# Kernel optimization log

Measured on AMD Instinct MI355X. Metric: run time of the kernel, lower is better.

## Reference

```python
import jax, jax.numpy as jnp
import numpy as np

K = 3            # kernel_size
ZETA = 1e-3      # crf_zeta
NUM_ITER = 2     # crf_num_iter
TOL = 0.0        # tolerance


def unfold3(x):
    """torch.nn.Unfold(3, stride=1, padding=1): [B,C,H,W] -> [B,C,9,H*W].
    Channel-major, kernel positions row-major (matches torch ordering)."""
    B, C, H, W = x.shape
    xp = jnp.pad(x, ((0, 0), (0, 0), (1, 1), (1, 1)))
    patches = jnp.stack(
        [xp[:, :, i:i + H, j:j + W] for i in range(K) for j in range(K)], axis=2
    )  # [B,C,9,H,W]
    return patches.reshape(B, C, K * K, H * W)


def setup_inputs() -> dict:
    key = jax.random.key(0)
    k1, k2, k3 = jax.random.split(key, 3)
    B, C, H, W, D = 2, 3, 256, 704, 64
    # scale color to O(zeta) so the gaussian affinity kernel is non-degenerate
    color = jax.random.normal(k1, (B, C, H, W), dtype=jnp.float32) * ZETA
    feats = jax.random.normal(k2, (B, C, H, W), dtype=jnp.float32)  # unused by forward, kept for signature fidelity
    logits = jax.random.normal(k3, (B, D, H, W), dtype=jnp.float32)
    ws = jnp.full((1,), 0.015, dtype=jnp.float32)  # learned weight self.ws[0]
    return {"color": color, "feats": feats, "logits": logits, "ws": ws}


def reference(color, feats, logits, ws):
    B, C, H, W = color.shape
    D = logits.shape[1]
    HW = H * W

    # gaussian affinity kernel from guide image: [B, 9, HW]
    uc = unfold3(color)  # [B,C,9,HW]
    kernel = jnp.exp(-(((uc - color.reshape(B, C, 1, HW)) ** 2)
                       / (2.0 * ZETA ** 2)).sum(1))

    # label compatibility matrix miu: [D, D]
    idx = jnp.arange(D)
    miu = jnp.clip(jnp.abs(idx[:, None] - idx[None, :]).astype(jnp.float32) - TOL, 0.0)

    logits_flat = logits.reshape(B, D, HW)
    q = jax.nn.softmax(logits, axis=1)
    for _ in range(NUM_ITER):
        uq = unfold3(q)  # [B,D,9,HW]
        q_tilde = (uq * kernel[:, None]).sum(2) * ws  # [B,D,HW]
        q_hat = jnp.einsum('de,ben->bdn', miu, q_tilde)  # [B,D,HW]
        q = jax.nn.softmax(logits_flat - q_hat, axis=1).reshape(B, D, H, W)
    return q
```

## Files before the change

### kernel.cpp

```cpp
#include <hip/hip_runtime.h>
#include <hip/hip_fp16.h>

#define HH 256
#define WW 704
#define DD 64
#define CC 3
#define BB 2
#define HWN (HH * WW)

#define TY 8
#define TX 16
#define RY0 12
#define RX0 20
#define NP0 (RY0 * RX0)
#define RY1 10
#define RX1 18
#define NP1 (RY1 * RX1)
#define NTX (WW / TX)
#define NTY (HH / TY)
#define NTILES (NTX * NTY)

static constexpr float INV2Z2 = 1.0f / (2.0f * 1e-3f * 1e-3f);

__global__ __launch_bounds__(256) void affinity_kernel(
    const float* __restrict__ color, const float* __restrict__ wsp,
    float* __restrict__ kaff)
{
    int n = blockIdx.x * 256 + threadIdx.x;
    int b = blockIdx.y;
    int h = n / WW, w = n - h * WW;
    float wsv = wsp[0];

    const float* cb = color + (size_t)b * CC * HWN + n;
    float c0 = cb[0], c1 = cb[HWN], c2 = cb[2 * HWN];
    bool hm = h > 0, hp = h < HH - 1, wm = w > 0, wp = w < WW - 1;

    float* kb = kaff + (size_t)b * 9 * HWN + n;
#pragma unroll
    for (int dh = -1; dh <= 1; ++dh) {
#pragma unroll
        for (int dw = -1; dw <= 1; ++dw) {
            int k = (dh + 1) * 3 + (dw + 1);
            bool valid = (dh < 0 ? hm : (dh > 0 ? hp : true)) &&
                         (dw < 0 ? wm : (dw > 0 ? wp : true));
            int off = valid ? (dh * WW + dw) : 0;
            float u0 = valid ? cb[off] : 0.f;
            float u1 = valid ? cb[HWN + off] : 0.f;
            float u2 = valid ? cb[2 * HWN + off] : 0.f;
            float d0 = u0 - c0, d1 = u1 - c1, d2 = u2 - c2;
            float ss = d0 * d0 + d1 * d1 + d2 * d2;
            kb[(size_t)k * HWN] = wsv * __expf(-ss * INV2Z2);
        }
    }
}

__device__ __forceinline__ void acc_tap(const unsigned* q, int p0, int cg,
                                        __half2 kh, __half2* tv2) {
    int ia = p0 * 32 + ((cg * 8) ^ ((p0 & 7) << 2));
    int ib = ia ^ 4;
    const __half2* qa = (const __half2*)&q[ia];
    const __half2* qb = (const __half2*)&q[ib];
    tv2[0] = __hfma2(kh, qa[0], tv2[0]);
    tv2[1] = __hfma2(kh, qa[1], tv2[1]);
    tv2[2] = __hfma2(kh, qa[2], tv2[2]);
    tv2[3] = __hfma2(kh, qa[3], tv2[3]);
    tv2[4] = __hfma2(kh, qb[0], tv2[4]);
    tv2[5] = __hfma2(kh, qb[1], tv2[5]);
    tv2[6] = __hfma2(kh, qb[2], tv2[6]);
    tv2[7] = __hfma2(kh, qb[3], tv2[7]);
}

__device__ __forceinline__ void pack_px(const float* u, float scale,
                                        uint4& a, uint4& bu) {
    __half2* pa = (__half2*)&a;
    __half2* pb = (__half2*)&bu;
    pa[0] = __floats2half2_rn(u[0]  * scale, u[1]  * scale);
    pa[1] = __floats2half2_rn(u[2]  * scale, u[3]  * scale);
    pa[2] = __floats2half2_rn(u[4]  * scale, u[5]  * scale);
    pa[3] = __floats2half2_rn(u[6]  * scale, u[7]  * scale);
    pb[0] = __floats2half2_rn(u[8]  * scale, u[9]  * scale);
    pb[1] = __floats2half2_rn(u[10] * scale, u[11] * scale);
    pb[2] = __floats2half2_rn(u[12] * scale, u[13] * scale);
    pb[3] = __floats2half2_rn(u[14] * scale, u[15] * scale);
}

__device__ __forceinline__ void st_raw(unsigned* q, int p, int cg,
                                       uint4 a, uint4 bu) {
    int ia = p * 32 + ((cg * 8) ^ ((p & 7) << 2));
    *(uint4*)&q[ia] = a;
    *(uint4*)&q[ia ^ 4] = bu;
}

__device__ __forceinline__ void st_px(unsigned* q, int p, int cg,
                                      const float* u, float scale) {
    uint4 a, bu;
    pack_px(u, scale, a, bu);
    st_raw(q, p, cg, a, bu);
}

__device__ __forceinline__ void scan4(float Aloc, float Bloc, int pxl, int cg,
                                      float& Ar, float& Br, float& T, float& E) {
    float A0 = __shfl(Aloc, pxl),      A1 = __shfl(Aloc, pxl + 16),
          A2 = __shfl(Aloc, pxl + 32), A3 = __shfl(Aloc, pxl + 48);
    float B0 = __shfl(Bloc, pxl),      B1 = __shfl(Bloc, pxl + 16),
          B2 = __shfl(Bloc, pxl + 32), B3 = __shfl(Bloc, pxl + 48);
    T = A0 + A1 + A2 + A3;  E = B0 + B1 + B2 + B3;
    Ar = 0.f; Br = 0.f;
    if (cg > 0) { Ar += A0; Br += B0; }
    if (cg > 1) { Ar += A1; Br += B1; }
    if (cg > 2) { Ar += A2; Br += B2; }
}

__device__ __forceinline__ float finish_px(float* tv, const float* lg,
                                           int pxl, int cg) {
    float Aloc = 0.f, Bloc = 0.f;
#pragma unroll
    for (int i = 0; i < 16; ++i) {
        float e = (float)(cg * 16 + i);
        Aloc += tv[i]; Bloc += e * tv[i];
    }
    float Ar, Br, T, E;
    scan4(Aloc, Bloc, pxl, cg, Ar, Br, T, E);
    float s = 0.f;
#pragma unroll
    for (int i = 0; i < 16; ++i) {
        float e = (float)(cg * 16 + i);
        Ar += tv[i]; Br += e * tv[i];
        float v = lg[(size_t)i * HWN] - (2.f * (e * Ar - Br) + E - e * T);
        tv[i] = __expf(v); s += tv[i];
    }
    s += __shfl_xor(s, 16);
    s += __shfl_xor(s, 32);
    return 1.f / s;
}

__device__ __forceinline__ void load_k(const float* kfb, int n, int gy, int gx,
                                       float* k) {
#pragma unroll
    for (int j = 0; j < 9; ++j) k[j] = kfb[(size_t)j * HWN + n];
    if (gy <= 0)      { k[0] = k[1] = k[2] = 0.f; }
    if (gy >= HH - 1) { k[6] = k[7] = k[8] = 0.f; }
    if (gx <= 0)      { k[0] = k[3] = k[6] = 0.f; }
    if (gx >= WW - 1) { k[2] = k[5] = k[8] = 0.f; }
}

__device__ __forceinline__ void stencil9(const unsigned* qs, int rowstride,
                                         int py, int px, int cg,
                                         const float* k, float* tv) {
    __half2 tv2[8];
#pragma unroll
    for (int j = 0; j < 8; ++j) tv2[j] = __float2half2_rn(0.f);
    int base = (py + 1) * rowstride + (px + 1);
#pragma unroll
    for (int tap = 0; tap < 9; ++tap) {
        int dy = tap / 3 - 1, dx = tap - (tap / 3) * 3 - 1;
        acc_tap(qs, base + dy * rowstride + dx, cg, __float2half2_rn(k[tap]), tv2);
    }
#pragma unroll
    for (int j = 0; j < 8; ++j) {
        float2 f = __half22float2(tv2[j]);
        tv[2 * j] = f.x; tv[2 * j + 1] = f.y;
    }
}

__global__ __launch_bounds__(512) void fused_crf_kernel(
    const float* __restrict__ logits, const float* __restrict__ kaff,
    float* __restrict__ qout)
{
    __shared__ unsigned qs[NP0 * 32];

    const int t = threadIdx.x;
    const int lane = t & 63;
    const int wv = t >> 6;
    const int pxl = lane & 15;
    const int cg = lane >> 4;
    const int b = blockIdx.y;
    const int tid16 = wv * 16 + pxl;

    const int bid = blockIdx.x;
    const int pb = (bid & 7) * (NTILES / 8) + (bid >> 3);
    const int tyr = pb / NTX, txc = pb - tyr * NTX;
    const int y0 = tyr * TY, x0 = txc * TX;

    const float* lgb = logits + ((size_t)b * DD + cg * 16) * HWN;
    const float* kfb = kaff + (size_t)b * 9 * HWN;

    for (int r = 0; r < 2; ++r) {
        int id = r * 128 + tid16;
        if (id < NP0) {
            int py = id / RX0, px = id - py * RX0;
            int gy = min(max(y0 - 2 + py, 0), HH - 1);
            int gx = min(max(x0 - 2 + px, 0), WW - 1);
            const float* lg = lgb + gy * WW + gx;
            float v[16];
            float s = 0.f;
#pragma unroll
            for (int i = 0; i < 16; ++i) {
                v[i] = __expf(lg[(size_t)i * HWN]);
                s += v[i];
            }
            s += __shfl_xor(s, 16);
            s += __shfl_xor(s, 32);
            st_px(qs, id, cg, v, 1.0f / s);
        }
    }
    __syncthreads();

    uint4 aA, buA;
    {
        int py = tid16 / RX1, px = tid16 - py * RX1;
        int gy = y0 - 1 + py, gx = x0 - 1 + px;
        int cy = min(max(gy, 0), HH - 1), cx = min(max(gx, 0), WW - 1);
        int n = cy * WW + cx;
        float k[9];
        load_k(kfb, n, gy, gx, k);
        float tv[16];
        stencil9(qs, RX0, py, px, cg, k, tv);
        float inv = finish_px(tv, lgb + n, pxl, cg);
        pack_px(tv, inv, aA, buA);
    }
    const int idB = 128 + tid16;
    const bool validB = idB < NP1;
    uint4 aB, buB;
    if (validB) {
        int py = idB / RX1, px = idB - py * RX1;
        int gy = y0 - 1 + py, gx = x0 - 1 + px;
        int cy = min(max(gy, 0), HH - 1), cx = min(max(gx, 0), WW - 1);
        int n = cy * WW + cx;
        float k[9];
        load_k(kfb, n, gy, gx, k);
        float tv[16];
        stencil9(qs, RX0, py, px, cg, k, tv);
        float inv = finish_px(tv, lgb + n, pxl, cg);
        pack_px(tv, inv, aB, buB);
    }
    __syncthreads();

    st_raw(qs, tid16, cg, aA, buA);
    if (validB) st_raw(qs, idB, cg, aB, buB);
    __syncthreads();

    {
        int py = tid16 >> 4, px = tid16 & 15;
        int gy = y0 + py, gx = x0 + px;
        int n = gy * WW + gx;

        float k[9];
        load_k(kfb, n, gy, gx, k);

        float tv[16];
        stencil9(qs, RX1, py, px, cg, k, tv);
        float inv = finish_px(tv, lgb + n, pxl, cg);

        float* qo = qout + ((size_t)b * DD + cg * 16) * HWN + n;
#pragma unroll
        for (int i = 0; i < 16; ++i) qo[(size_t)i * HWN] = tv[i] * inv;
    }
}

extern "C" void kernel_launch(void* const* d_in, const int* in_sizes, int n_in,
                              void* d_out, int out_size, void* d_ws, size_t ws_size,
                              hipStream_t stream) {
    const float* color  = (const float*)d_in[0];
    const float* logits = (const float*)d_in[2];
    const float* wsp    = (const float*)d_in[3];

    float* q_out = (float*)d_out;
    float* kaff  = (float*)d_ws;

    dim3 gridA(HWN / 256, BB);
    affinity_kernel<<<gridA, 256, 0, stream>>>(color, wsp, kaff);

    dim3 gridF(NTILES, BB);
    fused_crf_kernel<<<gridF, 512, 0, stream>>>(logits, kaff, q_out);
}
```

Measured before the change: 90.01 us.

## Replace per-iteration logits reloads with cached softmax times exp2 of message

Uses the identity softmax(logits - q_hat) ∝ softmax(logits) · exp(-q_hat). Both CRF iterations now multiply the initial fp16 softmax, already held in shared memory, by exp(-q_hat) instead of reloading 64 logits per pixel from global memory. The ws weight is pre-scaled by log2(e) so the exponent can use the hardware exp2 instruction. The centre q0 for the final stage is read from shared memory before the buffer is overwritten. This removes a large share of global read traffic, at the cost of using fp16-rounded q0 as the base, which loses some precision for very small probabilities.

```diff
diff --git a/kernel.cpp b/kernel.cpp
--- a/kernel.cpp
+++ b/kernel.cpp
@@ -21,6 +21,15 @@
 #define NTILES (NTX * NTY)
 
 static constexpr float INV2Z2 = 1.0f / (2.0f * 1e-3f * 1e-3f);
+static constexpr float LOG2E  = 1.4426950408889634f;
+
+__device__ __forceinline__ float fexp2(float x) {
+#if __has_builtin(__builtin_amdgcn_exp2f)
+    return __builtin_amdgcn_exp2f(x);
+#else
+    return __expf(x * 0.6931471805599453f);
+#endif
+}
 
 __global__ __launch_bounds__(256) void affinity_kernel(
     const float* __restrict__ color, const float* __restrict__ wsp,
@@ -29,7 +38,7 @@
     int n = blockIdx.x * 256 + threadIdx.x;
     int b = blockIdx.y;
     int h = n / WW, w = n - h * WW;
-    float wsv = wsp[0];
+    float wsv = wsp[0] * LOG2E;
 
     const float* cb = color + (size_t)b * CC * HWN + n;
     float c0 = cb[0], c1 = cb[HWN], c2 = cb[2 * HWN];
@@ -70,6 +79,28 @@
     tv2[7] = __hfma2(kh, qb[3], tv2[7]);
 }
 
+__device__ __forceinline__ void ld_raw(const unsigned* q, int p, int cg,
+                                       uint4& a, uint4& bu) {
+    int ia = p * 32 + ((cg * 8) ^ ((p & 7) << 2));
+    a  = *(const uint4*)&q[ia];
+    bu = *(const uint4*)&q[ia ^ 4];
+}
+
+__device__ __forceinline__ void unpack_px(uint4 a, uint4 bu, float* qc) {
+    const __half2* pa = (const __half2*)&a;
+    const __half2* pb = (const __half2*)&bu;
+#pragma unroll
+    for (int j = 0; j < 4; ++j) {
+        float2 f = __half22float2(pa[j]);
+        qc[2 * j] = f.x; qc[2 * j + 1] = f.y;
+    }
+#pragma unroll
+    for (int j = 0; j < 4; ++j) {
+        float2 f = __half22float2(pb[j]);
+        qc[8 + 2 * j] = f.x; qc[8 + 2 * j + 1] = f.y;
+    }
+}
+
 __device__ __forceinline__ void pack_px(const float* u, float scale,
                                         uint4& a, uint4& bu) {
     __half2* pa = (__half2*)&a;
@@ -111,8 +142,8 @@
     if (cg > 2) { Ar += A2; Br += B2; }
 }
 
-__device__ __forceinline__ float finish_px(float* tv, const float* lg,
-                                           int pxl, int cg) {
+__device__ __forceinline__ float finish_mult(float* tv, const float* qc,
+                                             int pxl, int cg) {
     float Aloc = 0.f, Bloc = 0.f;
 #pragma unroll
     for (int i = 0; i < 16; ++i) {
@@ -126,8 +157,9 @@
     for (int i = 0; i < 16; ++i) {
         float e = (float)(cg * 16 + i);
         Ar += tv[i]; Br += e * tv[i];
-        float v = lg[(size_t)i * HWN] - (2.f * (e * Ar - Br) + E - e * T);
-        tv[i] = __expf(v); s += tv[i];
+        float qh2 = 2.f * (e * Ar - Br) + E - e * T;
+        tv[i] = qc[i] * fexp2(-qh2);
+        s += tv[i];
     }
     s += __shfl_xor(s, 16);
     s += __shfl_xor(s, 32);
@@ -216,7 +248,11 @@
         load_k(kfb, n, gy, gx, k);
         float tv[16];
         stencil9(qs, RX0, py, px, cg, k, tv);
-        float inv = finish_px(tv, lgb + n, pxl, cg);
+        uint4 ca, cb2;
+        ld_raw(qs, (py + 1) * RX0 + (px + 1), cg, ca, cb2);
+        float qc[16];
+        unpack_px(ca, cb2, qc);
+        float inv = finish_mult(tv, qc, pxl, cg);
         pack_px(tv, inv, aA, buA);
     }
     const int idB = 128 + tid16;
@@ -231,8 +267,18 @@
         load_k(kfb, n, gy, gx, k);
         float tv[16];
         stencil9(qs, RX0, py, px, cg, k, tv);
-        float inv = finish_px(tv, lgb + n, pxl, cg);
+        uint4 ca, cb2;
+        ld_raw(qs, (py + 1) * RX0 + (px + 1), cg, ca, cb2);
+        float qc[16];
+        unpack_px(ca, cb2, qc);
+        float inv = finish_mult(tv, qc, pxl, cg);
         pack_px(tv, inv, aB, buB);
+    }
+
+    uint4 q0cA, q0cB;
+    {
+        int pyc = tid16 >> 4, pxc = tid16 & 15;
+        ld_raw(qs, (pyc + 2) * RX0 + (pxc + 2), cg, q0cA, q0cB);
     }
     __syncthreads();
 
@@ -250,7 +296,9 @@
 
         float tv[16];
         stencil9(qs, RX1, py, px, cg, k, tv);
-        float inv = finish_px(tv, lgb + n, pxl, cg);
+        float qc[16];
+        unpack_px(q0cA, q0cB, qc);
+        float inv = finish_mult(tv, qc, pxl, cg);
 
         float* qo = qout + ((size_t)b * DD + cg * 16) * HWN + n;
 #pragma unroll
```

Result: faster. 80.37 us (-10.7%).
